# Kernel optimization log

Hardware: AMD Instinct MI355X
Metric: run time of the kernel (lower is better)

The kernel has to match this reference:

```python
import jax, jax.numpy as jnp
import numpy as np

N_NODES = 100000
N_EDGES = 1600000
F_IN = 256
HID = 128
N_CLS = 64
K_APPNP = 10
ALPHA = 0.1


def setup_inputs() -> dict:
    key = jax.random.key(0)
    ks = jax.random.split(key, 12)
    x = jax.random.normal(ks[0], (N_NODES, F_IN), dtype=jnp.float32)
    edge_index = jax.random.randint(ks[1], (2, N_EDGES), 0, N_NODES, dtype=jnp.int64)
    def lin(k, fan_in, fan_out):
        s = 1.0 / np.sqrt(fan_in)
        kw, kb = jax.random.split(k)
        W = jax.random.uniform(kw, (fan_in, fan_out), minval=-s, maxval=s, dtype=jnp.float32)
        b = jax.random.uniform(kb, (fan_out,), minval=-s, maxval=s, dtype=jnp.float32)
        return W, b
    W1, b1 = lin(ks[2], F_IN, HID)
    W2, b2 = lin(ks[3], HID, HID)
    Wc, bc = lin(ks[4], HID, N_CLS)
    We, be = lin(ks[5], N_CLS, N_CLS)
    return {"x": x, "edge_index": edge_index, "W1": W1, "b1": b1, "W2": W2,
            "b2": b2, "Wc": Wc, "bc": bc, "We": We, "be": be}


def reference(x, edge_index, W1, b1, W2, b2, Wc, bc, We, be):
    N = x.shape[0]
    loop = jnp.arange(N)
    row = jnp.concatenate([edge_index[0], loop])  # source nodes (+ self loops)
    col = jnp.concatenate([edge_index[1], loop])  # target nodes (+ self loops)
    # symmetric GCN normalization: deg computed on targets
    deg = jax.ops.segment_sum(jnp.ones_like(col, dtype=x.dtype), col, num_segments=N)
    dinv = jnp.where(deg > 0, jax.lax.rsqrt(deg), 0.0)
    norm = dinv[row] * dinv[col]  # [E+N]

    def prop(h):  # normalized scatter-add aggregation
        return jax.ops.segment_sum(h[row] * norm[:, None], col, num_segments=N)

    # GCNConv: transform -> propagate -> bias (dropout is eval no-op)
    h = jax.nn.relu(prop(x @ W1) + b1)
    h = jax.nn.relu(prop(h @ W2) + b2)
    logits = h @ Wc + bc
    ev = jax.nn.relu(logits @ We + be)
    # APPNP: z_{k+1} = (1-alpha) * A_hat z_k + alpha * ev
    z = ev
    for _ in range(K_APPNP):
        z = (1.0 - ALPHA) * prop(z) + ALPHA * ev
    return jax.nn.log_softmax(z, axis=1)
```

## Files before the change

### kernel.cpp

```cpp
#include <hip/hip_runtime.h>
#include <hip/hip_fp16.h>


struct __align__(16) half8 { __half2 h[4]; };
typedef _Float16 f16x8 __attribute__((ext_vector_type(8)));
typedef float f32x4 __attribute__((ext_vector_type(4)));

__global__ __launch_bounds__(256) void k_init(int* deg, int* cursor, int N) {
    int i = blockIdx.x * 256 + threadIdx.x;
    if (i < N) { deg[i] = 1; cursor[i] = 0; }
}

__global__ __launch_bounds__(256) void k_count(const int* __restrict__ dst, int* deg, int E) {
    int e = blockIdx.x * 256 + threadIdx.x;
    if (e < E) atomicAdd(&deg[dst[e]], 1);
}

__global__ __launch_bounds__(256) void k_scanA(const int* __restrict__ deg, int* bs, int N) {
    __shared__ int s[256];
    int t = threadIdx.x;
    int i = blockIdx.x * 256 + t;
    int c = (i < N) ? (deg[i] - 1) : 0;
    s[t] = c; __syncthreads();
    for (int o = 128; o > 0; o >>= 1) {
        if (t < o) s[t] += s[t + o];
        __syncthreads();
    }
    if (t == 0) bs[blockIdx.x] = s[0];
}

__global__ __launch_bounds__(512) void k_scanB(int* bs, int NB) {
    __shared__ int s[512];
    int t = threadIdx.x;
    int v = (t < NB) ? bs[t] : 0;
    s[t] = v; __syncthreads();
    for (int o = 1; o < 512; o <<= 1) {
        int u = (t >= o) ? s[t - o] : 0;
        __syncthreads();
        s[t] += u;
        __syncthreads();
    }
    if (t < NB) bs[t] = s[t] - v;
}

__global__ __launch_bounds__(256) void k_scanC(const int* __restrict__ deg, const int* __restrict__ bs,
                                               int* row_ptr, float* dinv, int N) {
    __shared__ int s[256];
    int t = threadIdx.x;
    int i = blockIdx.x * 256 + t;
    int c = (i < N) ? (deg[i] - 1) : 0;
    s[t] = c; __syncthreads();
    for (int o = 1; o < 256; o <<= 1) {
        int u = (t >= o) ? s[t - o] : 0;
        __syncthreads();
        s[t] += u;
        __syncthreads();
    }
    if (i < N) {
        int off = bs[blockIdx.x];
        row_ptr[i] = off + s[t] - c;
        dinv[i] = rsqrtf((float)deg[i]);
        if (i == N - 1) row_ptr[N] = off + s[t];
    }
}

__global__ __launch_bounds__(256) void k_fill(const int* __restrict__ src, const int* __restrict__ dst,
                                              const int* __restrict__ row_ptr, int* cursor,
                                              int* csr_src, int E) {
    int e = blockIdx.x * 256 + threadIdx.x;
    if (e < E) {
        int d = dst[e];
        int pos = row_ptr[d] + atomicAdd(&cursor[d], 1);
        csr_src[pos] = src[e];
    }
}

__global__ __launch_bounds__(256) void k_fuseW(const float* __restrict__ Wc,
                                               const float* __restrict__ bc,
                                               const float* __restrict__ We,
                                               const float* __restrict__ be,
                                               float* __restrict__ Wf,
                                               float* __restrict__ bf) {
    __shared__ float sWe[64 * 64];
    int tid = threadIdx.x;
    for (int i = tid; i < 64 * 64 / 4; i += 256)
        ((float4*)sWe)[i] = ((const float4*)We)[i];
    __syncthreads();
    for (int idx = tid; idx < 128 * 64; idx += 256) {
        int r = idx >> 6, c = idx & 63;
        float s = 0.f;
#pragma unroll 8
        for (int j = 0; j < 64; j++) s += Wc[r * 64 + j] * sWe[j * 64 + c];
        Wf[idx] = s;
    }
    if (tid < 64) {
        float s = be[tid];
#pragma unroll 8
        for (int j = 0; j < 64; j++) s += bc[j] * sWe[j * 64 + tid];
        bf[tid] = s;
    }
}

__global__ __launch_bounds__(256) void k_prepW(const float* __restrict__ W,
                                               __half* __restrict__ Wt, int K) {
    int idx = blockIdx.x * 256 + threadIdx.x;
    if (idx < 128 * K) {
        int n = idx / K, k = idx % K;
        Wt[idx] = __float2half(W[k * 128 + n]);
    }
}

template <int K, bool IN_F16>
__global__ __launch_bounds__(256) void k_mfma_gemm(const void* __restrict__ Xv,
                                                   const __half* __restrict__ Wt,
                                                   const float* __restrict__ dinv,
                                                   __half* __restrict__ Y, int N) {
    constexpr int PAD = 8;
    constexpr int LDK = K + PAD;
    __shared__ __half sA[32 * LDK];
    int tid = threadIdx.x;
    int rowBase = blockIdx.x * 32;

    if (IN_F16) {
        const __half* X = (const __half*)Xv;
        constexpr int C8 = K / 8;
        for (int i = tid; i < 32 * C8; i += 256) {
            int r = i / C8, c8 = i % C8;
            int rg = rowBase + r; if (rg > N - 1) rg = N - 1;
            *(f16x8*)&sA[r * LDK + 8 * c8] = *(const f16x8*)&X[(long)rg * K + 8 * c8];
        }
    } else {
        const float* X = (const float*)Xv;
        constexpr int C4 = K / 4;
        for (int i = tid; i < 32 * C4; i += 256) {
            int r = i / C4, c4 = i % C4;
            int rg = rowBase + r; if (rg > N - 1) rg = N - 1;
            const float4 v = *(const float4*)&X[(long)rg * K + 4 * c4];
            __half2* dst = (__half2*)&sA[r * LDK + 4 * c4];
            dst[0] = __floats2half2_rn(v.x, v.y);
            dst[1] = __floats2half2_rn(v.z, v.w);
        }
    }
    __syncthreads();

    int wave = tid >> 6, lane = tid & 63;
    int m = lane & 15, quad = lane >> 4;
    int rw = (wave & 1) * 16;
    int cb = (wave >> 1) * 64;

    f32x4 d[4];
#pragma unroll
    for (int ct = 0; ct < 4; ct++) d[ct] = {0.f, 0.f, 0.f, 0.f};

#pragma unroll
    for (int kc = 0; kc < K / 32; kc++) {
        const f16x8 a = *(const f16x8*)&sA[(rw + m) * LDK + kc * 32 + quad * 8];
#pragma unroll
        for (int ct = 0; ct < 4; ct++) {
            const f16x8 b = *(const f16x8*)&Wt[(long)(cb + ct * 16 + m) * K + kc * 32 + quad * 8];
            d[ct] = __builtin_amdgcn_mfma_f32_16x16x32_f16(a, b, d[ct], 0, 0, 0);
        }
    }

#pragma unroll
    for (int ct = 0; ct < 4; ct++) {
        int col = cb + ct * 16 + m;
#pragma unroll
        for (int reg = 0; reg < 4; reg++) {
            int row = rowBase + rw + quad * 4 + reg;
            if (row < N)
                Y[(long)row * 128 + col] = __float2half(d[ct][reg] * dinv[row]);
        }
    }
}

__global__ __launch_bounds__(256) void k_cls(const float* __restrict__ H,
                                             const float* __restrict__ Wf,
                                             const float* __restrict__ bf,
                                             const float* __restrict__ dinv,
                                             float* __restrict__ ev,
                                             __half* __restrict__ evs, int N) {
    __shared__ float sH[32 * 128];
    int tid = threadIdx.x;
    long rowBase = (long)blockIdx.x * 32;
    const float4* xg = (const float4*)(H + rowBase * 128);
    for (int i = tid; i < 32 * 128 / 4; i += 256) ((float4*)sH)[i] = xg[i];
    __syncthreads();

    int col = tid & 63;
    int r0 = (tid >> 6) * 8;
    float acc[8];
#pragma unroll
    for (int r = 0; r < 8; r++) acc[r] = 0.f;

    for (int k = 0; k < 128; k += 4) {
        float w0 = Wf[(k + 0) * 64 + col];
        float w1 = Wf[(k + 1) * 64 + col];
        float w2 = Wf[(k + 2) * 64 + col];
        float w3 = Wf[(k + 3) * 64 + col];
#pragma unroll
        for (int r = 0; r < 8; r++) {
            const float4 xv = *(const float4*)&sH[(r0 + r) * 128 + k];
            acc[r] += xv.x * w0 + xv.y * w1 + xv.z * w2 + xv.w * w3;
        }
    }
    float b = bf[col];
#pragma unroll
    for (int r = 0; r < 8; r++) {
        long row = rowBase + r0 + r;
        float v = fmaxf(acc[r] + b, 0.f);
        ev[row * 64 + col] = v;
        evs[row * 64 + col] = __float2half(v * dinv[row]);
    }
}

template <int F, int MODE>
__global__ __launch_bounds__(256) void k_prop2(const __half* __restrict__ tab,
                                               const int* __restrict__ row_ptr,
                                               const int* __restrict__ csr_src,
                                               const float* __restrict__ dinv,
                                               const float* __restrict__ bias,
                                               const void* __restrict__ evx,
                                               void* __restrict__ out, int N) {
    constexpr int LPE = F / 8;
    constexpr int S = 64 / LPE;
    int wave = threadIdx.x >> 6;
    int lane = threadIdx.x & 63;
    int node = blockIdx.x * 4 + wave;
    if (node >= N) return;
    int slot = lane / LPE;
    int fl = lane % LPE;
    const int2 se = *(const int2*)&row_ptr[node];
    int s = se.x, e = se.y;

    float acc[8], accB[8];
#pragma unroll
    for (int q = 0; q < 8; q++) { acc[q] = 0.f; accB[q] = 0.f; }

    int j = s + slot;
    for (; j + S < e; j += 2 * S) {
        const half8 a = *(const half8*)&tab[(long)csr_src[j] * F + 8 * fl];
        const half8 b = *(const half8*)&tab[(long)csr_src[j + S] * F + 8 * fl];
#pragma unroll
        for (int q = 0; q < 4; q++) {
            float2 fa = __half22float2(a.h[q]);
            float2 fb = __half22float2(b.h[q]);
            acc[2 * q] += fa.x; acc[2 * q + 1] += fa.y;
            accB[2 * q] += fb.x; accB[2 * q + 1] += fb.y;
        }
    }
    if (j < e) {
        const half8 a = *(const half8*)&tab[(long)csr_src[j] * F + 8 * fl];
#pragma unroll
        for (int q = 0; q < 4; q++) {
            float2 fa = __half22float2(a.h[q]);
            acc[2 * q] += fa.x; acc[2 * q + 1] += fa.y;
        }
    }
    if (slot == 0) {
        const half8 a = *(const half8*)&tab[(long)node * F + 8 * fl];
#pragma unroll
        for (int q = 0; q < 4; q++) {
            float2 fa = __half22float2(a.h[q]);
            acc[2 * q] += fa.x; acc[2 * q + 1] += fa.y;
        }
    }
#pragma unroll
    for (int q = 0; q < 8; q++) acc[q] += accB[q];

#pragma unroll
    for (int off = LPE; off < 64; off <<= 1) {
#pragma unroll
        for (int q = 0; q < 8; q++) acc[q] += __shfl_xor(acc[q], off, 64);
    }

    if (slot == 0) {
        float di = dinv[node];
        if (MODE == 0) {
            const float4 b0 = *(const float4*)&bias[8 * fl];
            const float4 b1 = *(const float4*)&bias[8 * fl + 4];
            float* o = (float*)out + (long)node * F + 8 * fl;
            float4 v0, v1;
            v0.x = fmaxf(di * acc[0] + b0.x, 0.f);
            v0.y = fmaxf(di * acc[1] + b0.y, 0.f);
            v0.z = fmaxf(di * acc[2] + b0.z, 0.f);
            v0.w = fmaxf(di * acc[3] + b0.w, 0.f);
            v1.x = fmaxf(di * acc[4] + b1.x, 0.f);
            v1.y = fmaxf(di * acc[5] + b1.y, 0.f);
            v1.z = fmaxf(di * acc[6] + b1.z, 0.f);
            v1.w = fmaxf(di * acc[7] + b1.w, 0.f);
            *(float4*)o = v0;
            *(float4*)(o + 4) = v1;
        } else if (MODE == 3) {
            const float4 b0 = *(const float4*)&bias[8 * fl];
            const float4 b1 = *(const float4*)&bias[8 * fl + 4];
            half8 ov;
            ov.h[0] = __floats2half2_rn(fmaxf(di * acc[0] + b0.x, 0.f),
                                        fmaxf(di * acc[1] + b0.y, 0.f));
            ov.h[1] = __floats2half2_rn(fmaxf(di * acc[2] + b0.z, 0.f),
                                        fmaxf(di * acc[3] + b0.w, 0.f));
            ov.h[2] = __floats2half2_rn(fmaxf(di * acc[4] + b1.x, 0.f),
                                        fmaxf(di * acc[5] + b1.y, 0.f));
            ov.h[3] = __floats2half2_rn(fmaxf(di * acc[6] + b1.z, 0.f),
                                        fmaxf(di * acc[7] + b1.w, 0.f));
            *(half8*)&((__half*)out)[(long)node * F + 8 * fl] = ov;
        } else if (MODE == 1) {
            float d2 = 0.9f * di * di;
            const half8 eh = *(const half8*)&((const __half*)evx)[(long)node * F + 8 * fl];
            half8 ov;
#pragma unroll
            for (int q = 0; q < 4; q++) {
                float2 ef = __half22float2(eh.h[q]);
                float vx = d2 * acc[2 * q] + 0.1f * ef.x;
                float vy = d2 * acc[2 * q + 1] + 0.1f * ef.y;
                ov.h[q] = __floats2half2_rn(vx, vy);
            }
            *(half8*)&((__half*)out)[(long)node * F + 8 * fl] = ov;
        } else {
            float d1 = 0.9f * di;
            const float* ef = (const float*)evx + (long)node * F + 8 * fl;
            const float4 e0 = *(const float4*)ef;
            const float4 e1 = *(const float4*)(ef + 4);
            float v[8];
            v[0] = d1 * acc[0] + 0.1f * e0.x;
            v[1] = d1 * acc[1] + 0.1f * e0.y;
            v[2] = d1 * acc[2] + 0.1f * e0.z;
            v[3] = d1 * acc[3] + 0.1f * e0.w;
            v[4] = d1 * acc[4] + 0.1f * e1.x;
            v[5] = d1 * acc[5] + 0.1f * e1.y;
            v[6] = d1 * acc[6] + 0.1f * e1.z;
            v[7] = d1 * acc[7] + 0.1f * e1.w;
            float m = v[0];
#pragma unroll
            for (int q = 1; q < 8; q++) m = fmaxf(m, v[q]);
#pragma unroll
            for (int off = 1; off < LPE; off <<= 1) m = fmaxf(m, __shfl_xor(m, off, 64));
            float ssum = 0.f;
#pragma unroll
            for (int q = 0; q < 8; q++) ssum += __expf(v[q] - m);
#pragma unroll
            for (int off = 1; off < LPE; off <<= 1) ssum += __shfl_xor(ssum, off, 64);
            float lse = m + __logf(ssum);
            float* o = (float*)out + (long)node * F + 8 * fl;
            float4 v0, v1;
            v0.x = v[0] - lse; v0.y = v[1] - lse; v0.z = v[2] - lse; v0.w = v[3] - lse;
            v1.x = v[4] - lse; v1.y = v[5] - lse; v1.z = v[6] - lse; v1.w = v[7] - lse;
            *(float4*)o = v0;
            *(float4*)(o + 4) = v1;
        }
    }
}

extern "C" void kernel_launch(void* const* d_in, const int* in_sizes, int n_in,
                              void* d_out, int out_size, void* d_ws, size_t ws_size,
                              hipStream_t stream) {
    const float* x  = (const float*)d_in[0];
    const int* edges = (const int*)d_in[1];
    const float* W1 = (const float*)d_in[2];
    const float* b1 = (const float*)d_in[3];
    const float* W2 = (const float*)d_in[4];
    const float* b2 = (const float*)d_in[5];
    const float* Wc = (const float*)d_in[6];
    const float* bc = (const float*)d_in[7];
    const float* We = (const float*)d_in[8];
    const float* be = (const float*)d_in[9];

    const int N = in_sizes[0] / 256;
    const int E = in_sizes[1] / 2;
    const int* esrc = edges;
    const int* edst = edges + E;

    char* ws = (char*)d_ws;
    size_t off = 0;
    auto alloc = [&](size_t bytes) -> void* {
        void* p = ws + off;
        off += (bytes + 255) & ~(size_t)255;
        return p;
    };
    int*    deg     = (int*)alloc((size_t)N * 4);
    int*    cursor  = (int*)alloc((size_t)N * 4);
    int*    row_ptr = (int*)alloc((size_t)(N + 1) * 4);
    float*  dinv    = (float*)alloc((size_t)N * 4);
    int*    bs      = (int*)alloc(4096 * 4);
    int*    csr_src = (int*)alloc((size_t)E * 4);
    __half* P       = (__half*)alloc((size_t)N * 128 * 2);
    __half* Q16     = (__half*)alloc((size_t)N * 128 * 2);
    float*  Q       = (float*)alloc((size_t)N * 128 * 4);
    __half* zA      = (__half*)alloc((size_t)N * 64 * 2);
    __half* zB      = (__half*)alloc((size_t)N * 64 * 2);
    __half* evs     = (__half*)alloc((size_t)N * 64 * 2);
    float*  Wf      = (float*)alloc(128 * 64 * 4);
    float*  bf      = (float*)alloc(64 * 4);
    __half* W1t     = (__half*)alloc(128 * 256 * 2);
    __half* W2t     = (__half*)alloc(128 * 128 * 2);
    float*  ev      = (float*)d_out;

    const int nbN = (N + 255) / 256;
    const int nbE = (E + 255) / 256;
    const int nbP = (N + 3) / 4;
    const int nbG = (N + 31) / 32;

    k_init<<<nbN, 256, 0, stream>>>(deg, cursor, N);
    k_count<<<nbE, 256, 0, stream>>>(edst, deg, E);
    k_fuseW<<<1, 256, 0, stream>>>(Wc, bc, We, be, Wf, bf);
    k_prepW<<<(128 * 256 + 255) / 256, 256, 0, stream>>>(W1, W1t, 256);
    k_prepW<<<(128 * 128 + 255) / 256, 256, 0, stream>>>(W2, W2t, 128);
    k_scanA<<<nbN, 256, 0, stream>>>(deg, bs, N);
    k_scanB<<<1, 512, 0, stream>>>(bs, nbN);
    k_scanC<<<nbN, 256, 0, stream>>>(deg, bs, row_ptr, dinv, N);
    k_fill<<<nbE, 256, 0, stream>>>(esrc, edst, row_ptr, cursor, csr_src, E);

    k_mfma_gemm<256, false><<<nbG, 256, 0, stream>>>(x, W1t, dinv, P, N);
    k_prop2<128, 3><<<nbP, 256, 0, stream>>>(P, row_ptr, csr_src, dinv, b1, nullptr, Q16, N);

    k_mfma_gemm<128, true><<<nbG, 256, 0, stream>>>(Q16, W2t, dinv, P, N);
    k_prop2<128, 0><<<nbP, 256, 0, stream>>>(P, row_ptr, csr_src, dinv, b2, nullptr, Q, N);

    k_cls<<<N / 32, 256, 0, stream>>>(Q, Wf, bf, dinv, ev, evs, N);

    const __half* zin = evs;
    __half* zout;
    for (int it = 0; it < 9; ++it) {
        zout = (it % 2 == 0) ? zA : zB;
        k_prop2<64, 1><<<nbP, 256, 0, stream>>>(zin, row_ptr, csr_src, dinv, nullptr, evs, zout, N);
        zin = zout;
    }
    k_prop2<64, 2><<<nbP, 256, 0, stream>>>(zin, row_ptr, csr_src, dinv, nullptr, ev, (float*)d_out, N);
}
```

Before: 1.113 ms.

## Record edge rank in count pass, hoist GEMM weights to registers, fp16 layer-2 output

The degree-count atomic now returns each edge's slot within its target row, so the CSR fill pass no longer needs a second atomic on a cursor array and is a plain indexed scatter. It costs an extra E-sized rank buffer. The MFMA GEMM loads its weight fragments into registers before staging the A tile, with a launch-bounds occupancy hint. The second GCN propagation writes fp16 instead of fp32, and the classifier reads fp16, halving that intermediate's traffic at some precision cost.

```diff
diff --git a/kernel.cpp b/kernel.cpp
--- a/kernel.cpp
+++ b/kernel.cpp
@@ -6,14 +6,18 @@
 typedef _Float16 f16x8 __attribute__((ext_vector_type(8)));
 typedef float f32x4 __attribute__((ext_vector_type(4)));
 
-__global__ __launch_bounds__(256) void k_init(int* deg, int* cursor, int N) {
+__global__ __launch_bounds__(256) void k_init(int* deg, int N) {
     int i = blockIdx.x * 256 + threadIdx.x;
-    if (i < N) { deg[i] = 1; cursor[i] = 0; }
-}
-
-__global__ __launch_bounds__(256) void k_count(const int* __restrict__ dst, int* deg, int E) {
+    if (i < N) deg[i] = 1;
+}
+
+__global__ __launch_bounds__(256) void k_count(const int* __restrict__ dst,
+                                               int* deg, int* __restrict__ rank, int E) {
     int e = blockIdx.x * 256 + threadIdx.x;
-    if (e < E) atomicAdd(&deg[dst[e]], 1);
+    if (e < E) {
+        int r = atomicAdd(&deg[dst[e]], 1);
+        rank[e] = r - 1;
+    }
 }
 
 __global__ __launch_bounds__(256) void k_scanA(const int* __restrict__ deg, int* bs, int N) {
@@ -65,14 +69,11 @@
 }
 
 __global__ __launch_bounds__(256) void k_fill(const int* __restrict__ src, const int* __restrict__ dst,
-                                              const int* __restrict__ row_ptr, int* cursor,
-                                              int* csr_src, int E) {
+                                              const int* __restrict__ row_ptr,
+                                              const int* __restrict__ rank,
+                                              int* __restrict__ csr_src, int E) {
     int e = blockIdx.x * 256 + threadIdx.x;
-    if (e < E) {
-        int d = dst[e];
-        int pos = row_ptr[d] + atomicAdd(&cursor[d], 1);
-        csr_src[pos] = src[e];
-    }
+    if (e < E) csr_src[row_ptr[dst[e]] + rank[e]] = src[e];
 }
 
 __global__ __launch_bounds__(256) void k_fuseW(const float* __restrict__ Wc,
@@ -111,15 +112,26 @@
 }
 
 template <int K, bool IN_F16>
-__global__ __launch_bounds__(256) void k_mfma_gemm(const void* __restrict__ Xv,
-                                                   const __half* __restrict__ Wt,
-                                                   const float* __restrict__ dinv,
-                                                   __half* __restrict__ Y, int N) {
+__global__ __launch_bounds__(256, 2) void k_mfma_gemm(const void* __restrict__ Xv,
+                                                      const __half* __restrict__ Wt,
+                                                      const float* __restrict__ dinv,
+                                                      __half* __restrict__ Y, int N) {
     constexpr int PAD = 8;
     constexpr int LDK = K + PAD;
     __shared__ __half sA[32 * LDK];
     int tid = threadIdx.x;
     int rowBase = blockIdx.x * 32;
+    int wave = tid >> 6, lane = tid & 63;
+    int m = lane & 15, quad = lane >> 4;
+    int rw = (wave & 1) * 16;
+    int cb = (wave >> 1) * 64;
+
+    f16x8 bf[K / 32][4];
+#pragma unroll
+    for (int kc = 0; kc < K / 32; kc++)
+#pragma unroll
+        for (int ct = 0; ct < 4; ct++)
+            bf[kc][ct] = *(const f16x8*)&Wt[(long)(cb + ct * 16 + m) * K + kc * 32 + quad * 8];
 
     if (IN_F16) {
         const __half* X = (const __half*)Xv;
@@ -143,11 +155,6 @@
     }
     __syncthreads();
 
-    int wave = tid >> 6, lane = tid & 63;
-    int m = lane & 15, quad = lane >> 4;
-    int rw = (wave & 1) * 16;
-    int cb = (wave >> 1) * 64;
-
     f32x4 d[4];
 #pragma unroll
     for (int ct = 0; ct < 4; ct++) d[ct] = {0.f, 0.f, 0.f, 0.f};
@@ -156,10 +163,8 @@
     for (int kc = 0; kc < K / 32; kc++) {
         const f16x8 a = *(const f16x8*)&sA[(rw + m) * LDK + kc * 32 + quad * 8];
 #pragma unroll
-        for (int ct = 0; ct < 4; ct++) {
-            const f16x8 b = *(const f16x8*)&Wt[(long)(cb + ct * 16 + m) * K + kc * 32 + quad * 8];
-            d[ct] = __builtin_amdgcn_mfma_f32_16x16x32_f16(a, b, d[ct], 0, 0, 0);
-        }
+        for (int ct = 0; ct < 4; ct++)
+            d[ct] = __builtin_amdgcn_mfma_f32_16x16x32_f16(a, bf[kc][ct], d[ct], 0, 0, 0);
     }
 
 #pragma unroll
@@ -174,17 +179,17 @@
     }
 }
 
-__global__ __launch_bounds__(256) void k_cls(const float* __restrict__ H,
+__global__ __launch_bounds__(256) void k_cls(const __half* __restrict__ H,
                                              const float* __restrict__ Wf,
                                              const float* __restrict__ bf,
                                              const float* __restrict__ dinv,
                                              float* __restrict__ ev,
                                              __half* __restrict__ evs, int N) {
-    __shared__ float sH[32 * 128];
+    __shared__ __half sH[32 * 128];
     int tid = threadIdx.x;
     long rowBase = (long)blockIdx.x * 32;
-    const float4* xg = (const float4*)(H + rowBase * 128);
-    for (int i = tid; i < 32 * 128 / 4; i += 256) ((float4*)sH)[i] = xg[i];
+    const half8* xg = (const half8*)(H + rowBase * 128);
+    for (int i = tid; i < 32 * 128 / 8; i += 256) ((half8*)sH)[i] = xg[i];
     __syncthreads();
 
     int col = tid & 63;
@@ -200,8 +205,11 @@
         float w3 = Wf[(k + 3) * 64 + col];
 #pragma unroll
         for (int r = 0; r < 8; r++) {
-            const float4 xv = *(const float4*)&sH[(r0 + r) * 128 + k];
-            acc[r] += xv.x * w0 + xv.y * w1 + xv.z * w2 + xv.w * w3;
+            const __half2 h01 = *(const __half2*)&sH[(r0 + r) * 128 + k];
+            const __half2 h23 = *(const __half2*)&sH[(r0 + r) * 128 + k + 2];
+            float2 f01 = __half22float2(h01);
+            float2 f23 = __half22float2(h23);
+            acc[r] += f01.x * w0 + f01.y * w1 + f23.x * w2 + f23.y * w3;
         }
     }
     float b = bf[col];
@@ -276,22 +284,7 @@
 
     if (slot == 0) {
         float di = dinv[node];
-        if (MODE == 0) {
-            const float4 b0 = *(const float4*)&bias[8 * fl];
-            const float4 b1 = *(const float4*)&bias[8 * fl + 4];
-            float* o = (float*)out + (long)node * F + 8 * fl;
-            float4 v0, v1;
-            v0.x = fmaxf(di * acc[0] + b0.x, 0.f);
-            v0.y = fmaxf(di * acc[1] + b0.y, 0.f);
-            v0.z = fmaxf(di * acc[2] + b0.z, 0.f);
-            v0.w = fmaxf(di * acc[3] + b0.w, 0.f);
-            v1.x = fmaxf(di * acc[4] + b1.x, 0.f);
-            v1.y = fmaxf(di * acc[5] + b1.y, 0.f);
-            v1.z = fmaxf(di * acc[6] + b1.z, 0.f);
-            v1.w = fmaxf(di * acc[7] + b1.w, 0.f);
-            *(float4*)o = v0;
-            *(float4*)(o + 4) = v1;
-        } else if (MODE == 3) {
+        if (MODE == 3) {
             const float4 b0 = *(const float4*)&bias[8 * fl];
             const float4 b1 = *(const float4*)&bias[8 * fl + 4];
             half8 ov;
@@ -378,14 +371,13 @@
         return p;
     };
     int*    deg     = (int*)alloc((size_t)N * 4);
-    int*    cursor  = (int*)alloc((size_t)N * 4);
     int*    row_ptr = (int*)alloc((size_t)(N + 1) * 4);
     float*  dinv    = (float*)alloc((size_t)N * 4);
     int*    bs      = (int*)alloc(4096 * 4);
+    int*    rank    = (int*)alloc((size_t)E * 4);
     int*    csr_src = (int*)alloc((size_t)E * 4);
     __half* P       = (__half*)alloc((size_t)N * 128 * 2);
     __half* Q16     = (__half*)alloc((size_t)N * 128 * 2);
-    float*  Q       = (float*)alloc((size_t)N * 128 * 4);
     __half* zA      = (__half*)alloc((size_t)N * 64 * 2);
     __half* zB      = (__half*)alloc((size_t)N * 64 * 2);
     __half* evs     = (__half*)alloc((size_t)N * 64 * 2);
@@ -400,23 +392,23 @@
     const int nbP = (N + 3) / 4;
     const int nbG = (N + 31) / 32;
 
-    k_init<<<nbN, 256, 0, stream>>>(deg, cursor, N);
-    k_count<<<nbE, 256, 0, stream>>>(edst, deg, E);
+    k_init<<<nbN, 256, 0, stream>>>(deg, N);
+    k_count<<<nbE, 256, 0, stream>>>(edst, deg, rank, E);
     k_fuseW<<<1, 256, 0, stream>>>(Wc, bc, We, be, Wf, bf);
     k_prepW<<<(128 * 256 + 255) / 256, 256, 0, stream>>>(W1, W1t, 256);
     k_prepW<<<(128 * 128 + 255) / 256, 256, 0, stream>>>(W2, W2t, 128);
     k_scanA<<<nbN, 256, 0, stream>>>(deg, bs, N);
     k_scanB<<<1, 512, 0, stream>>>(bs, nbN);
     k_scanC<<<nbN, 256, 0, stream>>>(deg, bs, row_ptr, dinv, N);
-    k_fill<<<nbE, 256, 0, stream>>>(esrc, edst, row_ptr, cursor, csr_src, E);
+    k_fill<<<nbE, 256, 0, stream>>>(esrc, edst, row_ptr, rank, csr_src, E);
 
     k_mfma_gemm<256, false><<<nbG, 256, 0, stream>>>(x, W1t, dinv, P, N);
     k_prop2<128, 3><<<nbP, 256, 0, stream>>>(P, row_ptr, csr_src, dinv, b1, nullptr, Q16, N);
 
     k_mfma_gemm<128, true><<<nbG, 256, 0, stream>>>(Q16, W2t, dinv, P, N);
-    k_prop2<128, 0><<<nbP, 256, 0, stream>>>(P, row_ptr, csr_src, dinv, b2, nullptr, Q, N);
-
-    k_cls<<<N / 32, 256, 0, stream>>>(Q, Wf, bf, dinv, ev, evs, N);
+    k_prop2<128, 3><<<nbP, 256, 0, stream>>>(P, row_ptr, csr_src, dinv, b2, nullptr, Q16, N);
+
+    k_cls<<<N / 32, 256, 0, stream>>>(Q16, Wf, bf, dinv, ev, evs, N);
 
     const __half* zin = evs;
     __half* zout;
```

New measurement: 1.079 ms. 1.03x faster.
